# Kernel tuning notes

Hardware: AMD Instinct MI355X
Metric: run time of the kernel (lower is better)

## Reference

```python
import jax, jax.numpy as jnp
import numpy as np

N = 100000   # nodes
E = 1600000  # edges
F = 64       # input node features
H = 64       # hidden dim
G = 512      # graphs in batch


def setup_inputs() -> dict:
    key = jax.random.key(0)
    ks = jax.random.split(key, 10)
    x = jax.random.normal(ks[0], (N, F), dtype=jnp.float32)
    edge_index = jax.random.randint(ks[1], (2, E), 0, N, dtype=jnp.int32)
    batch = jnp.sort(jax.random.randint(ks[2], (N,), 0, G, dtype=jnp.int32))
    s = 1.0 / np.sqrt(H)
    W1 = jax.random.normal(ks[3], (F, H), dtype=jnp.float32) * s
    b1 = jnp.zeros((H,), jnp.float32)
    W2 = jax.random.normal(ks[4], (H, H), dtype=jnp.float32) * s
    b2 = jnp.zeros((H,), jnp.float32)
    W3 = jax.random.normal(ks[5], (H, H), dtype=jnp.float32) * s
    b3 = jnp.zeros((H,), jnp.float32)
    return {"x": x, "edge_index": edge_index, "batch": batch,
            "W1": W1, "b1": b1, "W2": W2, "b2": b2, "W3": W3, "b3": b3}


def _gcn_conv(x, W, b, src, dst, dinv):
    # PyG GCNConv: h = x @ W; aggregate with sym-normalized adjacency incl. self-loops; + bias
    h = x @ W                                  # [N, H]
    norm = dinv[src] * dinv[dst]               # [E]
    agg = jax.ops.segment_sum(h[src] * norm[:, None], dst, num_segments=N)
    agg = agg + h * (dinv * dinv)[:, None]     # self-loop contribution
    return agg + b


def reference(x, edge_index, batch, W1, b1, W2, b2, W3, b3):
    src, dst = edge_index[0], edge_index[1]
    # degree with self-loops (counted on dst, as in PyG)
    deg = jax.ops.segment_sum(jnp.ones((E,), x.dtype), dst, num_segments=N) + 1.0
    dinv = jax.lax.rsqrt(deg)
    h = jax.nn.relu(_gcn_conv(x, W1, b1, src, dst, dinv))
    h = jax.nn.relu(_gcn_conv(h, W2, b2, src, dst, dinv))
    h = _gcn_conv(h, W3, b3, src, dst, dinv)
    # global mean pool over graphs
    sums = jax.ops.segment_sum(h, batch, num_segments=G)          # [G, H]
    cnts = jax.ops.segment_sum(jnp.ones((N,), h.dtype), batch, num_segments=G)
    return sums / jnp.maximum(cnts, 1.0)[:, None]
```

## Files before the change

kernel.cpp:

```cpp
#include <hip/hip_runtime.h>

#define N_NODES 100000
#define N_EDGES 1600000
#define FDIM 64
#define NGRAPH 512
#define NB 782
#define NBP 784
#define NWG 512
#define CHUNK 3125
#define DWG 64
#define DCHUNK ((N_NODES + DWG - 1) / DWG)
#define MAXD 128

__device__ __forceinline__ unsigned short f2bf(float v) {
    unsigned int x = __float_as_uint(v);
    x += 0x7FFF + ((x >> 16) & 1);
    return (unsigned short)(x >> 16);
}

__global__ void scan_block(const int* __restrict__ in, int* __restrict__ excl,
                           int* __restrict__ blocksums, int n) {
    __shared__ int lds[256];
    int t = threadIdx.x;
    int base = blockIdx.x * 1024 + t * 4;
    int v0 = (base     < n) ? in[base]     : 0;
    int v1 = (base + 1 < n) ? in[base + 1] : 0;
    int v2 = (base + 2 < n) ? in[base + 2] : 0;
    int v3 = (base + 3 < n) ? in[base + 3] : 0;
    int s = v0 + v1 + v2 + v3;
    lds[t] = s;
    __syncthreads();
    for (int off = 1; off < 256; off <<= 1) {
        int x = (t >= off) ? lds[t - off] : 0;
        __syncthreads();
        lds[t] += x;
        __syncthreads();
    }
    int thrExcl = lds[t] - s;
    if (t == 255) blocksums[blockIdx.x] = lds[255];
    if (base     < n) excl[base]     = thrExcl;
    if (base + 1 < n) excl[base + 1] = thrExcl + v0;
    if (base + 2 < n) excl[base + 2] = thrExcl + v0 + v1;
    if (base + 3 < n) excl[base + 3] = thrExcl + v0 + v1 + v2;
}

__global__ void scan_top2(int* __restrict__ blocksums, int nb) {
    __shared__ int lds[256];
    int t = threadIdx.x;
    int base = t * 4;
    int v0 = (base     < nb) ? blocksums[base]     : 0;
    int v1 = (base + 1 < nb) ? blocksums[base + 1] : 0;
    int v2 = (base + 2 < nb) ? blocksums[base + 2] : 0;
    int v3 = (base + 3 < nb) ? blocksums[base + 3] : 0;
    int s = v0 + v1 + v2 + v3;
    lds[t] = s;
    __syncthreads();
    for (int off = 1; off < 256; off <<= 1) {
        int x = (t >= off) ? lds[t - off] : 0;
        __syncthreads();
        lds[t] += x;
        __syncthreads();
    }
    int excl = lds[t] - s;
    if (base     < nb) blocksums[base]     = excl;
    if (base + 1 < nb) blocksums[base + 1] = excl + v0;
    if (base + 2 < nb) blocksums[base + 2] = excl + v0 + v1;
    if (base + 3 < nb) blocksums[base + 3] = excl + v0 + v1 + v2;
}

__global__ void scan_add(int* __restrict__ out, const int* __restrict__ blocksums, int n) {
    int i = blockIdx.x * blockDim.x + threadIdx.x;
    if (i < n) out[i] += blocksums[i >> 10];
}

__global__ __launch_bounds__(256) void scan_single(int* __restrict__ data, int n) {
    __shared__ int lds[256];
    int t = threadIdx.x;
    int loc[32];
    int base = t * 32;
    int s = 0;
    #pragma unroll
    for (int j = 0; j < 32; ++j) { loc[j] = (base + j < n) ? data[base + j] : 0; s += loc[j]; }
    lds[t] = s;
    __syncthreads();
    for (int off = 1; off < 256; off <<= 1) {
        int x = (t >= off) ? lds[t - off] : 0;
        __syncthreads();
        lds[t] += x;
        __syncthreads();
    }
    int run = lds[t] - s;
    #pragma unroll
    for (int j = 0; j < 32; ++j) {
        int v = loc[j];
        if (base + j < n) data[base + j] = run;
        run += v;
    }
}

__global__ __launch_bounds__(256) void transpose_k(const int* __restrict__ src, int* __restrict__ dst,
                                                   int R, int C, int spitch, int dpitch) {
    __shared__ int tile[32][33];
    int tilesC = (C + 31) >> 5;
    int bx = blockIdx.x % tilesC;
    int by = blockIdx.x / tilesC;
    int tx = threadIdx.x & 31, ty = threadIdx.x >> 5;
    int c = bx * 32 + tx;
    #pragma unroll
    for (int j = 0; j < 32; j += 8) {
        int r = by * 32 + ty + j;
        if (r < R && c < C) tile[ty + j][tx] = src[r * spitch + c];
    }
    __syncthreads();
    int rT = by * 32 + tx;
    #pragma unroll
    for (int j = 0; j < 32; j += 8) {
        int cT = bx * 32 + ty + j;
        if (cT < C && rT < R) dst[cT * dpitch + rT] = tile[tx][ty + j];
    }
}

__global__ __launch_bounds__(256) void hist_kernel(const int* __restrict__ dst,
                                                   int* __restrict__ histWG, int E) {
    __shared__ int h[NB];
    int t = threadIdx.x, wg = blockIdx.x;
    for (int i = t; i < NB; i += 256) h[i] = 0;
    __syncthreads();
    int beg = wg * CHUNK, end = min(beg + CHUNK, E);
    for (int i = beg + t; i < end; i += 256) atomicAdd(&h[dst[i] >> 7], 1);
    __syncthreads();
    for (int i = t; i < NB; i += 256) histWG[wg * NBP + i] = h[i];
}

__global__ __launch_bounds__(256) void bin_kernel(const int* __restrict__ src,
                                                  const int* __restrict__ dst,
                                                  const int* __restrict__ baseWG,
                                                  int* __restrict__ ebin, int E) {
    __shared__ int base[NB];
    __shared__ int cur[NB];
    int t = threadIdx.x, wg = blockIdx.x;
    for (int i = t; i < NB; i += 256) { base[i] = baseWG[wg * NBP + i]; cur[i] = 0; }
    __syncthreads();
    int beg = wg * CHUNK, end = min(beg + CHUNK, E);
    for (int i = beg + t * 2; i < end; i += 512) {
        int d0 = dst[i], s0 = src[i];
        int b0 = d0 >> 7;
        int p0 = base[b0] + atomicAdd(&cur[b0], 1);
        ebin[p0] = ((d0 & 127) << 17) | s0;
        if (i + 1 < end) {
            int d1 = dst[i + 1], s1 = src[i + 1];
            int b1 = d1 >> 7;
            int p1 = base[b1] + atomicAdd(&cur[b1], 1);
            ebin[p1] = ((d1 & 127) << 17) | s1;
        }
    }
}

__global__ __launch_bounds__(256) void csr_sort2(const int* __restrict__ ebin,
                                                 const int* __restrict__ scannedT,
                                                 int* __restrict__ csr_src,
                                                 int* __restrict__ offsets,
                                                 float* __restrict__ dinv, int E) {
    __shared__ int cnt[128];
    __shared__ int seg[128];
    __shared__ int cur[128];
    __shared__ int buf[4352];
    int t = threadIdx.x, b = blockIdx.x;
    int nbase = b << 7;
    int nodes = min(128, N_NODES - nbase);
    int bstart = scannedT[b * NWG];
    int bend = (b == NB - 1) ? E : scannedT[(b + 1) * NWG];
    if (t < 128) cnt[t] = 0;
    __syncthreads();
    for (int i = bstart + t; i < bend; i += 256) atomicAdd(&cnt[ebin[i] >> 17], 1);
    __syncthreads();
    if (t < 128) seg[t] = cnt[t];
    __syncthreads();
    for (int off = 1; off < 128; off <<= 1) {
        int v = 0;
        if (t < 128 && t >= off) v = seg[t - off];
        __syncthreads();
        if (t < 128) seg[t] += v;
        __syncthreads();
    }
    if (t < nodes) {
        int excl = seg[t] - cnt[t];
        offsets[nbase + t] = bstart + excl;
        dinv[nbase + t] = rsqrtf((float)cnt[t] + 1.0f);
        cur[t] = excl;
    }
    if (b == 0 && t == 0) offsets[N_NODES] = E;
    __syncthreads();
    for (int i = bstart + t; i < bend; i += 256) {
        int v = ebin[i];
        int p = atomicAdd(&cur[v >> 17], 1);
        buf[p] = v & 0x1FFFF;
    }
    __syncthreads();
    int span = bend - bstart;
    for (int i = t; i < span; i += 256) csr_src[bstart + i] = buf[i];
}

__global__ __launch_bounds__(256) void histD_kernel(const int* __restrict__ offsets,
                                                    int* __restrict__ histD) {
    __shared__ int h[MAXD];
    int t = threadIdx.x, wg = blockIdx.x;
    if (t < MAXD) h[t] = 0;
    __syncthreads();
    int beg = wg * DCHUNK, end = min(beg + DCHUNK, N_NODES);
    for (int i = beg + t; i < end; i += 256) {
        int d = min(offsets[i + 1] - offsets[i], MAXD - 1);
        atomicAdd(&h[d], 1);
    }
    __syncthreads();
    if (t < MAXD) histD[t * DWG + wg] = h[t];
}

__global__ __launch_bounds__(256) void binD_kernel(const int* __restrict__ offsets,
                                                   const int* __restrict__ scannedD,
                                                   int* __restrict__ perm) {
    __shared__ int base[MAXD];
    __shared__ int cur[MAXD];
    int t = threadIdx.x, wg = blockIdx.x;
    if (t < MAXD) { base[t] = scannedD[t * DWG + wg]; cur[t] = 0; }
    __syncthreads();
    int beg = wg * DCHUNK, end = min(beg + DCHUNK, N_NODES);
    for (int i = beg + t; i < end; i += 256) {
        int d = min(offsets[i + 1] - offsets[i], MAXD - 1);
        int pos = base[d] + atomicAdd(&cur[d], 1);
        perm[pos] = i;
    }
}

__global__ __launch_bounds__(256) void gemm64(const float* __restrict__ X,
                                              const float* __restrict__ W,
                                              const float* __restrict__ dinv,
                                              unsigned short* __restrict__ Hout, int n) {
    __shared__ float Ws[64 * 68];
    __shared__ float Xs[64 * 68];
    int t = threadIdx.x;
    int r0 = blockIdx.x * 64;

    #pragma unroll
    for (int kk = 0; kk < 16; ++kk) {
        int idx = t + kk * 256;
        int r = idx >> 6, c = idx & 63;
        Ws[r * 68 + c] = W[idx];
        float v = (r0 + r < n) ? X[(size_t)(r0 + r) * FDIM + c] : 0.0f;
        Xs[c * 68 + r] = v;
    }
    __syncthreads();

    int rg = (t >> 4) << 2;
    int cg = (t & 15) << 2;
    float4 acc0 = {0, 0, 0, 0}, acc1 = {0, 0, 0, 0};
    float4 acc2 = {0, 0, 0, 0}, acc3 = {0, 0, 0, 0};

    #pragma unroll 8
    for (int k = 0; k < 64; ++k) {
        float4 xv = *(const float4*)&Xs[k * 68 + rg];
        float4 wv = *(const float4*)&Ws[k * 68 + cg];
        acc0.x += xv.x * wv.x; acc0.y += xv.x * wv.y; acc0.z += xv.x * wv.z; acc0.w += xv.x * wv.w;
        acc1.x += xv.y * wv.x; acc1.y += xv.y * wv.y; acc1.z += xv.y * wv.z; acc1.w += xv.y * wv.w;
        acc2.x += xv.z * wv.x; acc2.y += xv.z * wv.y; acc2.z += xv.z * wv.z; acc2.w += xv.z * wv.w;
        acc3.x += xv.w * wv.x; acc3.y += xv.w * wv.y; acc3.z += xv.w * wv.z; acc3.w += xv.w * wv.w;
    }

    float4 accs[4] = {acc0, acc1, acc2, acc3};
    #pragma unroll
    for (int i = 0; i < 4; ++i) {
        int row = r0 + rg + i;
        if (row < n) {
            float sc = dinv[row];
            unsigned int u0 = (unsigned int)f2bf(accs[i].x * sc) | ((unsigned int)f2bf(accs[i].y * sc) << 16);
            unsigned int u1 = (unsigned int)f2bf(accs[i].z * sc) | ((unsigned int)f2bf(accs[i].w * sc) << 16);
            *(uint2*)&Hout[(size_t)row * FDIM + cg] = make_uint2(u0, u1);
        }
    }
}

__global__ __launch_bounds__(256) void gather_pn(const unsigned short* __restrict__ hs,
                                                 const int* __restrict__ csr_src,
                                                 const int* __restrict__ offsets,
                                                 const int* __restrict__ perm,
                                                 const float* __restrict__ dinv,
                                                 const float* __restrict__ bias,
                                                 float* __restrict__ outb,
                                                 int n, int do_relu) {
    int slot = (blockIdx.x * 256 + threadIdx.x) >> 3;
    int p = threadIdx.x & 7;
    if (slot >= n) return;
    int node = perm[slot];
    int beg = offsets[node], end = offsets[node + 1];

    float a0 = 0, a1 = 0, a2 = 0, a3 = 0, a4 = 0, a5 = 0, a6 = 0, a7 = 0;
    int k = beg;
    for (; k + 3 < end; k += 4) {
        int s0 = csr_src[k], s1 = csr_src[k + 1], s2 = csr_src[k + 2], s3 = csr_src[k + 3];
        uint4 v0 = *(const uint4*)(hs + ((size_t)s0 << 6) + (p << 3));
        uint4 v1 = *(const uint4*)(hs + ((size_t)s1 << 6) + (p << 3));
        uint4 v2 = *(const uint4*)(hs + ((size_t)s2 << 6) + (p << 3));
        uint4 v3 = *(const uint4*)(hs + ((size_t)s3 << 6) + (p << 3));
        a0 += __uint_as_float(v0.x << 16); a1 += __uint_as_float(v0.x & 0xFFFF0000u);
        a2 += __uint_as_float(v0.y << 16); a3 += __uint_as_float(v0.y & 0xFFFF0000u);
        a4 += __uint_as_float(v0.z << 16); a5 += __uint_as_float(v0.z & 0xFFFF0000u);
        a6 += __uint_as_float(v0.w << 16); a7 += __uint_as_float(v0.w & 0xFFFF0000u);
        a0 += __uint_as_float(v1.x << 16); a1 += __uint_as_float(v1.x & 0xFFFF0000u);
        a2 += __uint_as_float(v1.y << 16); a3 += __uint_as_float(v1.y & 0xFFFF0000u);
        a4 += __uint_as_float(v1.z << 16); a5 += __uint_as_float(v1.z & 0xFFFF0000u);
        a6 += __uint_as_float(v1.w << 16); a7 += __uint_as_float(v1.w & 0xFFFF0000u);
        a0 += __uint_as_float(v2.x << 16); a1 += __uint_as_float(v2.x & 0xFFFF0000u);
        a2 += __uint_as_float(v2.y << 16); a3 += __uint_as_float(v2.y & 0xFFFF0000u);
        a4 += __uint_as_float(v2.z << 16); a5 += __uint_as_float(v2.z & 0xFFFF0000u);
        a6 += __uint_as_float(v2.w << 16); a7 += __uint_as_float(v2.w & 0xFFFF0000u);
        a0 += __uint_as_float(v3.x << 16); a1 += __uint_as_float(v3.x & 0xFFFF0000u);
        a2 += __uint_as_float(v3.y << 16); a3 += __uint_as_float(v3.y & 0xFFFF0000u);
        a4 += __uint_as_float(v3.z << 16); a5 += __uint_as_float(v3.z & 0xFFFF0000u);
        a6 += __uint_as_float(v3.w << 16); a7 += __uint_as_float(v3.w & 0xFFFF0000u);
    }
    for (; k < end; ++k) {
        int s0 = csr_src[k];
        uint4 v0 = *(const uint4*)(hs + ((size_t)s0 << 6) + (p << 3));
        a0 += __uint_as_float(v0.x << 16); a1 += __uint_as_float(v0.x & 0xFFFF0000u);
        a2 += __uint_as_float(v0.y << 16); a3 += __uint_as_float(v0.y & 0xFFFF0000u);
        a4 += __uint_as_float(v0.z << 16); a5 += __uint_as_float(v0.z & 0xFFFF0000u);
        a6 += __uint_as_float(v0.w << 16); a7 += __uint_as_float(v0.w & 0xFFFF0000u);
    }
    uint4 sv = *(const uint4*)(hs + ((size_t)node << 6) + (p << 3));
    float dd = dinv[node];
    int fb = p << 3;
    const float4* bp = (const float4*)(bias + fb);
    float4 bv0 = bp[0], bv1 = bp[1];
    float o0 = dd * (a0 + __uint_as_float(sv.x << 16))        + bv0.x;
    float o1 = dd * (a1 + __uint_as_float(sv.x & 0xFFFF0000u)) + bv0.y;
    float o2 = dd * (a2 + __uint_as_float(sv.y << 16))        + bv0.z;
    float o3 = dd * (a3 + __uint_as_float(sv.y & 0xFFFF0000u)) + bv0.w;
    float o4 = dd * (a4 + __uint_as_float(sv.z << 16))        + bv1.x;
    float o5 = dd * (a5 + __uint_as_float(sv.z & 0xFFFF0000u)) + bv1.y;
    float o6 = dd * (a6 + __uint_as_float(sv.w << 16))        + bv1.z;
    float o7 = dd * (a7 + __uint_as_float(sv.w & 0xFFFF0000u)) + bv1.w;
    if (do_relu) {
        o0 = fmaxf(o0, 0.0f); o1 = fmaxf(o1, 0.0f); o2 = fmaxf(o2, 0.0f); o3 = fmaxf(o3, 0.0f);
        o4 = fmaxf(o4, 0.0f); o5 = fmaxf(o5, 0.0f); o6 = fmaxf(o6, 0.0f); o7 = fmaxf(o7, 0.0f);
    }
    float4* op = (float4*)(outb + (size_t)node * FDIM + fb);
    op[0] = make_float4(o0, o1, o2, o3);
    op[1] = make_float4(o4, o5, o6, o7);
}

__global__ void gstart_kernel(const int* __restrict__ batch, int* __restrict__ gstart, int n) {
    int g = blockIdx.x * blockDim.x + threadIdx.x;
    if (g > NGRAPH) return;
    if (g == NGRAPH) { gstart[NGRAPH] = n; return; }
    int lo = 0, hi = n;
    while (lo < hi) {
        int mid = (lo + hi) >> 1;
        if (batch[mid] < g) lo = mid + 1; else hi = mid;
    }
    gstart[g] = lo;
}

__global__ __launch_bounds__(256) void pool2(const float* __restrict__ h,
                                             const int* __restrict__ gstart,
                                             float* __restrict__ out) {
    __shared__ float red[4][64];
    int g = blockIdx.x;
    int beg = gstart[g], end = gstart[g + 1];
    int w = threadIdx.x >> 6, lane = threadIdx.x & 63;
    float acc = 0.0f;
    for (int i = beg + w; i < end; i += 4)
        acc += h[(size_t)i * FDIM + lane];
    red[w][lane] = acc;
    __syncthreads();
    if (w == 0) {
        float tot = red[0][lane] + red[1][lane] + red[2][lane] + red[3][lane];
        float cnt = (float)(end - beg);
        out[(size_t)g * FDIM + lane] = tot / fmaxf(cnt, 1.0f);
    }
}

extern "C" void kernel_launch(void* const* d_in, const int* in_sizes, int n_in,
                              void* d_out, int out_size, void* d_ws, size_t ws_size,
                              hipStream_t stream) {
    const float* x     = (const float*)d_in[0];
    const int*   ei    = (const int*)d_in[1];
    const int*   batch = (const int*)d_in[2];
    const float* W1    = (const float*)d_in[3];
    const float* b1    = (const float*)d_in[4];
    const float* W2    = (const float*)d_in[5];
    const float* b2    = (const float*)d_in[6];
    const float* W3    = (const float*)d_in[7];
    const float* b3    = (const float*)d_in[8];
    float* out = (float*)d_out;

    const int N = N_NODES, E = N_EDGES;
    const int* src = ei;
    const int* dst = ei + E;

    char* ws = (char*)d_ws;
    float*          dinv    = (float*)         (ws + 0);
    int*            offsets = (int*)           (ws + 400128);
    int*            csr_src = (int*)           (ws + 800256);
    float*          bufA    = (float*)         (ws + 7200384);
    unsigned short* hbf     = (unsigned short*)(ws + 32800384);
    int*            gstart  = (int*)           (ws + 45600384);
    int*            perm    = (int*)           (ws + 45602560);
    int*            scannedD= (int*)           (ws + 46002688);
    int* histT      = (int*)(ws + 7200384);
    int* blocksumsH = (int*)(ws + 8803328);
    int* histWG     = (int*)(ws + 8805376);
    int* ebin       = (int*)(ws + 10411520);

    hist_kernel<<<NWG, 256, 0, stream>>>(dst, histWG, E);
    {
        int tilesC = (NB + 31) / 32, tilesR = (NWG + 31) / 32;
        transpose_k<<<tilesC * tilesR, 256, 0, stream>>>(histWG, histT, NWG, NB, NBP, NWG);
    }
    const int nH = NB * NWG;
    const int nScanH = (nH + 1023) / 1024;
    scan_block<<<nScanH, 256, 0, stream>>>(histT, histT, blocksumsH, nH);
    scan_top2<<<1, 256, 0, stream>>>(blocksumsH, nScanH);
    scan_add<<<(nH + 255) / 256, 256, 0, stream>>>(histT, blocksumsH, nH);
    {
        int tilesC = (NWG + 31) / 32, tilesR = (NB + 31) / 32;
        transpose_k<<<tilesC * tilesR, 256, 0, stream>>>(histT, histWG, NB, NWG, NWG, NBP);
    }
    bin_kernel<<<NWG, 256, 0, stream>>>(src, dst, histWG, ebin, E);
    csr_sort2<<<NB, 256, 0, stream>>>(ebin, histT, csr_src, offsets, dinv, E);

    histD_kernel<<<DWG, 256, 0, stream>>>(offsets, scannedD);
    scan_single<<<1, 256, 0, stream>>>(scannedD, MAXD * DWG);
    binD_kernel<<<DWG, 256, 0, stream>>>(offsets, scannedD, perm);

    gstart_kernel<<<3, 256, 0, stream>>>(batch, gstart, N);

    const int gemmGrid   = (N + 63) / 64;
    const int gatherGrid = (N * 8 + 255) / 256;

    gemm64<<<gemmGrid, 256, 0, stream>>>(x, W1, dinv, hbf, N);
    gather_pn<<<gatherGrid, 256, 0, stream>>>(hbf, csr_src, offsets, perm, dinv, b1, bufA, N, 1);

    gemm64<<<gemmGrid, 256, 0, stream>>>(bufA, W2, dinv, hbf, N);
    gather_pn<<<gatherGrid, 256, 0, stream>>>(hbf, csr_src, offsets, perm, dinv, b2, bufA, N, 1);

    gemm64<<<gemmGrid, 256, 0, stream>>>(bufA, W3, dinv, hbf, N);
    gather_pn<<<gatherGrid, 256, 0, stream>>>(hbf, csr_src, offsets, perm, dinv, b3, bufA, N, 0);

    pool2<<<NGRAPH, 256, 0, stream>>>(bufA, gstart, out);
}
```

Before: 272.1 us.

## Fuse final GCN aggregation with mean pooling via bucketed edge scatter

```diff
diff --git a/kernel.cpp b/kernel.cpp
--- a/kernel.cpp
+++ b/kernel.cpp
@@ -11,12 +11,15 @@
 #define DWG 64
 #define DCHUNK ((N_NODES + DWG - 1) / DWG)
 #define MAXD 128
+#define GMAX 8
 
 __device__ __forceinline__ unsigned short f2bf(float v) {
     unsigned int x = __float_as_uint(v);
     x += 0x7FFF + ((x >> 16) & 1);
     return (unsigned short)(x >> 16);
 }
+#define BFLO(u) __uint_as_float((u) << 16)
+#define BFHI(u) __uint_as_float((u) & 0xFFFF0000u)
 
 __global__ void scan_block(const int* __restrict__ in, int* __restrict__ excl,
                            int* __restrict__ blocksums, int n) {
@@ -279,6 +282,10 @@
     }
 }
 
+#define ACC8(v) do { \
+    a0 += BFLO(v.x); a1 += BFHI(v.x); a2 += BFLO(v.y); a3 += BFHI(v.y); \
+    a4 += BFLO(v.z); a5 += BFHI(v.z); a6 += BFLO(v.w); a7 += BFHI(v.w); } while (0)
+
 __global__ __launch_bounds__(256) void gather_pn(const unsigned short* __restrict__ hs,
                                                  const int* __restrict__ csr_src,
                                                  const int* __restrict__ offsets,
@@ -295,50 +302,46 @@
 
     float a0 = 0, a1 = 0, a2 = 0, a3 = 0, a4 = 0, a5 = 0, a6 = 0, a7 = 0;
     int k = beg;
+    for (; k + 7 < end; k += 8) {
+        int s0 = csr_src[k],     s1 = csr_src[k + 1], s2 = csr_src[k + 2], s3 = csr_src[k + 3];
+        int s4 = csr_src[k + 4], s5 = csr_src[k + 5], s6 = csr_src[k + 6], s7 = csr_src[k + 7];
+        uint4 v0 = *(const uint4*)(hs + ((size_t)s0 << 6) + (p << 3));
+        uint4 v1 = *(const uint4*)(hs + ((size_t)s1 << 6) + (p << 3));
+        uint4 v2 = *(const uint4*)(hs + ((size_t)s2 << 6) + (p << 3));
+        uint4 v3 = *(const uint4*)(hs + ((size_t)s3 << 6) + (p << 3));
+        uint4 v4 = *(const uint4*)(hs + ((size_t)s4 << 6) + (p << 3));
+        uint4 v5 = *(const uint4*)(hs + ((size_t)s5 << 6) + (p << 3));
+        uint4 v6 = *(const uint4*)(hs + ((size_t)s6 << 6) + (p << 3));
+        uint4 v7 = *(const uint4*)(hs + ((size_t)s7 << 6) + (p << 3));
+        ACC8(v0); ACC8(v1); ACC8(v2); ACC8(v3);
+        ACC8(v4); ACC8(v5); ACC8(v6); ACC8(v7);
+    }
     for (; k + 3 < end; k += 4) {
         int s0 = csr_src[k], s1 = csr_src[k + 1], s2 = csr_src[k + 2], s3 = csr_src[k + 3];
         uint4 v0 = *(const uint4*)(hs + ((size_t)s0 << 6) + (p << 3));
         uint4 v1 = *(const uint4*)(hs + ((size_t)s1 << 6) + (p << 3));
         uint4 v2 = *(const uint4*)(hs + ((size_t)s2 << 6) + (p << 3));
         uint4 v3 = *(const uint4*)(hs + ((size_t)s3 << 6) + (p << 3));
-        a0 += __uint_as_float(v0.x << 16); a1 += __uint_as_float(v0.x & 0xFFFF0000u);
-        a2 += __uint_as_float(v0.y << 16); a3 += __uint_as_float(v0.y & 0xFFFF0000u);
-        a4 += __uint_as_float(v0.z << 16); a5 += __uint_as_float(v0.z & 0xFFFF0000u);
-        a6 += __uint_as_float(v0.w << 16); a7 += __uint_as_float(v0.w & 0xFFFF0000u);
-        a0 += __uint_as_float(v1.x << 16); a1 += __uint_as_float(v1.x & 0xFFFF0000u);
-        a2 += __uint_as_float(v1.y << 16); a3 += __uint_as_float(v1.y & 0xFFFF0000u);
-        a4 += __uint_as_float(v1.z << 16); a5 += __uint_as_float(v1.z & 0xFFFF0000u);
-        a6 += __uint_as_float(v1.w << 16); a7 += __uint_as_float(v1.w & 0xFFFF0000u);
-        a0 += __uint_as_float(v2.x << 16); a1 += __uint_as_float(v2.x & 0xFFFF0000u);
-        a2 += __uint_as_float(v2.y << 16); a3 += __uint_as_float(v2.y & 0xFFFF0000u);
-        a4 += __uint_as_float(v2.z << 16); a5 += __uint_as_float(v2.z & 0xFFFF0000u);
-        a6 += __uint_as_float(v2.w << 16); a7 += __uint_as_float(v2.w & 0xFFFF0000u);
-        a0 += __uint_as_float(v3.x << 16); a1 += __uint_as_float(v3.x & 0xFFFF0000u);
-        a2 += __uint_as_float(v3.y << 16); a3 += __uint_as_float(v3.y & 0xFFFF0000u);
-        a4 += __uint_as_float(v3.z << 16); a5 += __uint_as_float(v3.z & 0xFFFF0000u);
-        a6 += __uint_as_float(v3.w << 16); a7 += __uint_as_float(v3.w & 0xFFFF0000u);
+        ACC8(v0); ACC8(v1); ACC8(v2); ACC8(v3);
     }
     for (; k < end; ++k) {
         int s0 = csr_src[k];
         uint4 v0 = *(const uint4*)(hs + ((size_t)s0 << 6) + (p << 3));
-        a0 += __uint_as_float(v0.x << 16); a1 += __uint_as_float(v0.x & 0xFFFF0000u);
-        a2 += __uint_as_float(v0.y << 16); a3 += __uint_as_float(v0.y & 0xFFFF0000u);
-        a4 += __uint_as_float(v0.z << 16); a5 += __uint_as_float(v0.z & 0xFFFF0000u);
-        a6 += __uint_as_float(v0.w << 16); a7 += __uint_as_float(v0.w & 0xFFFF0000u);
+        ACC8(v0);
     }
     uint4 sv = *(const uint4*)(hs + ((size_t)node << 6) + (p << 3));
     float dd = dinv[node];
     int fb = p << 3;
     const float4* bp = (const float4*)(bias + fb);
     float4 bv0 = bp[0], bv1 = bp[1];
-    float o0 = dd * (a0 + __uint_as_float(sv.x << 16))        + bv0.x;
-    float o1 = dd * (a1 + __uint_as_float(sv.x & 0xFFFF0000u)) + bv0.y;
-    float o2 = dd * (a2 + __uint_as_float(sv.y << 16))        + bv0.z;
-    float o3 = dd * (a3 + __uint_as_float(sv.y & 0xFFFF0000u)) + bv0.w;
-    float o4 = dd * (a4 + __uint_as_float(sv.z << 16))        + bv1.x;
-    float o5 = dd * (a5 + __uint_as_float(sv.z & 0xFFFF0000u)) + bv1.y;
-    float o6 = dd * (a6 + __uint_as_float(sv.w << 16))        + bv1.z;
-    float o7 = dd * (a7 + __uint_as_float(sv.w & 0xFFFF0000u)) + bv1.w;
+    float o0 = dd * (a0 + BFLO(sv.x)) + bv0.x;
+    float o1 = dd * (a1 + BFHI(sv.x)) + bv0.y;
+    float o2 = dd * (a2 + BFLO(sv.y)) + bv0.z;
+    float o3 = dd * (a3 + BFHI(sv.y)) + bv0.w;
+    float o4 = dd * (a4 + BFLO(sv.z)) + bv1.x;
+    float o5 = dd * (a5 + BFHI(sv.z)) + bv1.y;
+    float o6 = dd * (a6 + BFLO(sv.w)) + bv1.z;
+    float o7 = dd * (a7 + BFHI(sv.w)) + bv1.w;
     if (do_relu) {
         o0 = fmaxf(o0, 0.0f); o1 = fmaxf(o1, 0.0f); o2 = fmaxf(o2, 0.0f); o3 = fmaxf(o3, 0.0f);
         o4 = fmaxf(o4, 0.0f); o5 = fmaxf(o5, 0.0f); o6 = fmaxf(o6, 0.0f); o7 = fmaxf(o7, 0.0f);
@@ -346,6 +349,113 @@
     float4* op = (float4*)(outb + (size_t)node * FDIM + fb);
     op[0] = make_float4(o0, o1, o2, o3);
     op[1] = make_float4(o4, o5, o6, o7);
+}
+
+__global__ __launch_bounds__(256) void gather_pool(const unsigned short* __restrict__ zs,
+                                                   const int* __restrict__ ebin,
+                                                   const int* __restrict__ bucketBase,
+                                                   const float* __restrict__ dinv,
+                                                   const int* __restrict__ batch,
+                                                   float* __restrict__ tpool, int E) {
+    __shared__ float dinv_l[128];
+    __shared__ int   gl[128];
+    __shared__ float tg[GMAX][64];
+    __shared__ int   gmin_s;
+    int t = threadIdx.x;
+    int b = blockIdx.x >> 1;
+    int half = blockIdx.x & 1;
+    int nbase = b << 7;
+    int nodes = min(128, N_NODES - nbase);
+    int bstart = bucketBase[b * NWG];
+    int bend   = (b == NB - 1) ? E : bucketBase[(b + 1) * NWG];
+
+    if (t == 0) gmin_s = batch[nbase];
+    for (int i = t; i < GMAX * 64; i += 256) ((float*)tg)[i] = 0.0f;
+    __syncthreads();
+    int gmin = gmin_s;
+    if (t < 128) {
+        dinv_l[t] = (t < nodes) ? dinv[nbase + t] : 0.0f;
+        gl[t]     = (t < nodes) ? (batch[nbase + t] - gmin) : 0;
+    }
+    __syncthreads();
+
+    int s = t >> 3, p = t & 7;
+    float a0[8], a1[8];
+    #pragma unroll
+    for (int j = 0; j < 8; ++j) { a0[j] = 0.0f; a1[j] = 0.0f; }
+
+    int span = bend - bstart;
+    int hbeg = bstart + half * (span >> 1);
+    int hend = (half == 0) ? (bstart + (span >> 1)) : bend;
+
+    for (int e = hbeg + s; e < hend; e += 32) {
+        int v = ebin[e];
+        int l = v >> 17;
+        int srcn = v & 0x1FFFF;
+        uint4 r = *(const uint4*)(zs + ((size_t)srcn << 6) + (p << 3));
+        float w = dinv_l[l];
+        int g = gl[l];
+        float f0 = BFLO(r.x), f1 = BFHI(r.x), f2 = BFLO(r.y), f3 = BFHI(r.y);
+        float f4 = BFLO(r.z), f5 = BFHI(r.z), f6 = BFLO(r.w), f7 = BFHI(r.w);
+        float w0 = (g == 0) ? w : 0.0f;
+        float w1 = (g == 1) ? w : 0.0f;
+        a0[0] += w0 * f0; a0[1] += w0 * f1; a0[2] += w0 * f2; a0[3] += w0 * f3;
+        a0[4] += w0 * f4; a0[5] += w0 * f5; a0[6] += w0 * f6; a0[7] += w0 * f7;
+        a1[0] += w1 * f0; a1[1] += w1 * f1; a1[2] += w1 * f2; a1[3] += w1 * f3;
+        a1[4] += w1 * f4; a1[5] += w1 * f5; a1[6] += w1 * f6; a1[7] += w1 * f7;
+        if (g >= 2) {
+            atomicAdd(&tg[g][p * 8 + 0], w * f0); atomicAdd(&tg[g][p * 8 + 1], w * f1);
+            atomicAdd(&tg[g][p * 8 + 2], w * f2); atomicAdd(&tg[g][p * 8 + 3], w * f3);
+            atomicAdd(&tg[g][p * 8 + 4], w * f4); atomicAdd(&tg[g][p * 8 + 5], w * f5);
+            atomicAdd(&tg[g][p * 8 + 6], w * f6); atomicAdd(&tg[g][p * 8 + 7], w * f7);
+        }
+    }
+
+    for (int l = half * 64 + s; l < min(nodes, half * 64 + 64); l += 32) {
+        uint4 r = *(const uint4*)(zs + ((size_t)(nbase + l) << 6) + (p << 3));
+        float w = dinv_l[l];
+        int g = gl[l];
+        float f0 = BFLO(r.x), f1 = BFHI(r.x), f2 = BFLO(r.y), f3 = BFHI(r.y);
+        float f4 = BFLO(r.z), f5 = BFHI(r.z), f6 = BFLO(r.w), f7 = BFHI(r.w);
+        float w0 = (g == 0) ? w : 0.0f;
+        float w1 = (g == 1) ? w : 0.0f;
+        a0[0] += w0 * f0; a0[1] += w0 * f1; a0[2] += w0 * f2; a0[3] += w0 * f3;
+        a0[4] += w0 * f4; a0[5] += w0 * f5; a0[6] += w0 * f6; a0[7] += w0 * f7;
+        a1[0] += w1 * f0; a1[1] += w1 * f1; a1[2] += w1 * f2; a1[3] += w1 * f3;
+        a1[4] += w1 * f4; a1[5] += w1 * f5; a1[6] += w1 * f6; a1[7] += w1 * f7;
+        if (g >= 2) {
+            atomicAdd(&tg[g][p * 8 + 0], w * f0); atomicAdd(&tg[g][p * 8 + 1], w * f1);
+            atomicAdd(&tg[g][p * 8 + 2], w * f2); atomicAdd(&tg[g][p * 8 + 3], w * f3);
+            atomicAdd(&tg[g][p * 8 + 4], w * f4); atomicAdd(&tg[g][p * 8 + 5], w * f5);
+            atomicAdd(&tg[g][p * 8 + 6], w * f6); atomicAdd(&tg[g][p * 8 + 7], w * f7);
+        }
+    }
+
+    #pragma unroll
+    for (int j = 0; j < 8; ++j) {
+        if (a0[j] != 0.0f) atomicAdd(&tg[0][p * 8 + j], a0[j]);
+        if (a1[j] != 0.0f) atomicAdd(&tg[1][p * 8 + j], a1[j]);
+    }
+    __syncthreads();
+
+    for (int i = t; i < GMAX * 64; i += 256) {
+        float v = ((float*)tg)[i];
+        if (v != 0.0f) {
+            int slot2 = i >> 6, c = i & 63;
+            int g = gmin + slot2;
+            if (g < NGRAPH) atomicAdd(&tpool[g * 64 + c], v);
+        }
+    }
+}
+
+__global__ void finalize_pool(const float* __restrict__ tpool, const int* __restrict__ gstart,
+                              const float* __restrict__ bias, float* __restrict__ out) {
+    int i = blockIdx.x * 256 + threadIdx.x;
+    if (i < NGRAPH * 64) {
+        int g = i >> 6, c = i & 63;
+        float cnt = (float)(gstart[g + 1] - gstart[g]);
+        out[i] = tpool[i] / fmaxf(cnt, 1.0f) + bias[c];
+    }
 }
 
 __global__ void gstart_kernel(const int* __restrict__ batch, int* __restrict__ gstart, int n) {
@@ -358,25 +468,6 @@
         if (batch[mid] < g) lo = mid + 1; else hi = mid;
     }
     gstart[g] = lo;
-}
-
-__global__ __launch_bounds__(256) void pool2(const float* __restrict__ h,
-                                             const int* __restrict__ gstart,
-                                             float* __restrict__ out) {
-    __shared__ float red[4][64];
-    int g = blockIdx.x;
-    int beg = gstart[g], end = gstart[g + 1];
-    int w = threadIdx.x >> 6, lane = threadIdx.x & 63;
-    float acc = 0.0f;
-    for (int i = beg + w; i < end; i += 4)
-        acc += h[(size_t)i * FDIM + lane];
-    red[w][lane] = acc;
-    __syncthreads();
-    if (w == 0) {
-        float tot = red[0][lane] + red[1][lane] + red[2][lane] + red[3][lane];
-        float cnt = (float)(end - beg);
-        out[(size_t)g * FDIM + lane] = tot / fmaxf(cnt, 1.0f);
-    }
 }
 
 extern "C" void kernel_launch(void* const* d_in, const int* in_sizes, int n_in,
@@ -406,10 +497,11 @@
     int*            gstart  = (int*)           (ws + 45600384);
     int*            perm    = (int*)           (ws + 45602560);
     int*            scannedD= (int*)           (ws + 46002688);
-    int* histT      = (int*)(ws + 7200384);
-    int* blocksumsH = (int*)(ws + 8803328);
-    int* histWG     = (int*)(ws + 8805376);
-    int* ebin       = (int*)(ws + 10411520);
+    float*          tpool   = (float*)         (ws + 46035712);
+    int*            histT   = (int*)           (ws + 46166784);
+    int*            histWG  = (int*)           (ws + 47768320);
+    int*            blocksumsH = (int*)        (ws + 49373952);
+    int*            ebin    = (int*)           (ws + 49376000);
 
     hist_kernel<<<NWG, 256, 0, stream>>>(dst, histWG, E);
     {
@@ -433,6 +525,7 @@
     binD_kernel<<<DWG, 256, 0, stream>>>(offsets, scannedD, perm);
 
     gstart_kernel<<<3, 256, 0, stream>>>(batch, gstart, N);
+    hipMemsetAsync(tpool, 0, (size_t)NGRAPH * FDIM * sizeof(float), stream);
 
     const int gemmGrid   = (N + 63) / 64;
     const int gatherGrid = (N * 8 + 255) / 256;
@@ -444,7 +537,6 @@
     gather_pn<<<gatherGrid, 256, 0, stream>>>(hbf, csr_src, offsets, perm, dinv, b2, bufA, N, 1);
 
     gemm64<<<gemmGrid, 256, 0, stream>>>(bufA, W3, dinv, hbf, N);
-    gather_pn<<<gatherGrid, 256, 0, stream>>>(hbf, csr_src, offsets, perm, dinv, b3, bufA, N, 0);
-
-    pool2<<<NGRAPH, 256, 0, stream>>>(bufA, gstart, out);
-}
+    gather_pool<<<NB * 2, 256, 0, stream>>>(hbf, ebin, histT, dinv, batch, tpool, E);
+    finalize_pool<<<(NGRAPH * FDIM + 255) / 256, 256, 0, stream>>>(tpool, gstart, b3, out);
+}
```

Measured after the change: 275.9 us. About the same (+1.4%).
